# Kernel optimization log

Measured on AMD Instinct MI355X. Metric: run time of the kernel, lower is better.

Reference implementation:

```python
import jax, jax.numpy as jnp
import numpy as np

T, B, E = 2048, 2, 1024
H, R = 16, 8
HD = E // H          # head_dim = 64
VD = E // R          # value_dim = attn_dim // num_rules = 128 (attn_dim = embed_dim)
SEL = E // H         # selection_dim = 64


def _linear_params(key, out_dim, in_dim):
    kw, kb = jax.random.split(key)
    lim = float(np.sqrt(6.0 / (in_dim + out_dim)))  # xavier_uniform
    W = jax.random.uniform(kw, (out_dim, in_dim), jnp.float32, -lim, lim)
    b = jnp.zeros((out_dim,), jnp.float32)
    return W, b


def setup_inputs() -> dict:
    key = jax.random.key(0)
    ks = jax.random.split(key, 7)
    query = jax.random.normal(ks[0], (T, B, E), jnp.float32)
    Wq, bq = _linear_params(ks[1], E, E)
    Wk, bk = _linear_params(ks[2], E, E)
    Wv, bv = _linear_params(ks[3], E, E)          # v_proj: embed_dim -> attn_dim (=E)
    Wvq, bvq = _linear_params(ks[4], SEL * H, E)  # value_q (q_compose=False)
    Wsc, bsc = _linear_params(ks[5], 1, SEL + VD) # score_network (nonlinear=False)
    Wo, bo = _linear_params(ks[6], E, H * VD)     # out_proj
    return {"query": query, "Wq": Wq, "bq": bq, "Wk": Wk, "bk": bk,
            "Wv": Wv, "bv": bv, "Wvq": Wvq, "bvq": bvq,
            "Wsc": Wsc, "bsc": bsc, "Wo": Wo, "bo": bo}


def reference(query, Wq, bq, Wk, bk, Wv, bv, Wvq, bvq, Wsc, bsc, Wo, bo):
    t, b, e = query.shape
    scaling = HD ** -0.5
    # projections (self-attention: k, v from query)
    q = (query @ Wq.T + bq) * scaling                       # (T,B,E)
    k = query @ Wk.T + bk                                   # (T,B,E)
    v = query @ Wv.T + bv                                   # (T,B,attn_dim)
    q = q.reshape(t, b, H, HD).transpose(1, 2, 0, 3)        # (B,H,T,HD)
    k = k.reshape(t, b, H, HD).transpose(1, 2, 0, 3)        # (B,H,S,HD)
    v = v.reshape(t, b, R, VD).transpose(1, 2, 0, 3)        # (B,R,S,VD)
    # standard multi-head search: softmax over source positions
    probs = jax.nn.softmax(jnp.einsum('bhtd,bhsd->bhts', q, k), axis=-1)
    # per-(head, rule) retrieved values
    attn = jnp.einsum('bhts,brsd->bhtrd', probs, v)         # (B,H,T,R,VD)
    # selection query from raw input (q_compose=False)
    v_q = (query @ Wvq.T + bvq).reshape(t, b, H, SEL).transpose(1, 2, 0, 3)  # (B,H,T,SEL)
    v_q = jnp.broadcast_to(v_q[:, :, :, None, :], (b, H, t, R, SEL))
    comp = jnp.concatenate([v_q, attn], axis=-1)            # (B,H,T,R,SEL+VD)
    score = comp @ Wsc.T + bsc                              # (B,H,T,R,1)
    sel = jax.nn.softmax(score, axis=3)                     # softmax over rules
    out = jnp.sum(attn * sel, axis=3)                       # (B,H,T,VD)
    out = out.transpose(2, 0, 1, 3).reshape(t, b, H * VD)   # (T,B,H*VD)
    return out @ Wo.T + bo                                  # (T,B,E)
```

## Files before the change

### kernel.cpp

```cpp
#include <hip/hip_runtime.h>
#include <hip/hip_bf16.h>
#include <stdint.h>

typedef unsigned short u16;
typedef unsigned int u32;
typedef __attribute__((ext_vector_type(8))) short bf16x8;
typedef __attribute__((ext_vector_type(4))) float f32x4;

#define TT 2048
#define BB 2
#define HH 16
#define RR 8
#define SS 2048
#define MROWS 4096

__device__ __forceinline__ float bf2f(u16 h){ union { u32 u; float f; } v; v.u = ((u32)h) << 16; return v.f; }
__device__ __forceinline__ u16 f2bf(float f){ union { float f; u32 u; } v; v.f = f; return (u16)((v.u + 0x7FFFu + ((v.u >> 16) & 1u)) >> 16); }
__device__ __forceinline__ void gl_lds16(const void* g, void* l){
  __builtin_amdgcn_global_load_lds((const __attribute__((address_space(1))) u32*)g,
                                   (__attribute__((address_space(3))) u32*)l, 16, 0, 0);
}

__global__ void k_cvt(const float* __restrict__ s, u16* __restrict__ d, int n, float scale){
  int i = blockIdx.x * blockDim.x + threadIdx.x;
  int st = gridDim.x * blockDim.x;
  for (; i < n; i += st) d[i] = f2bf(s[i] * scale);
}

__global__ void k_bias(const float* __restrict__ bq, const float* __restrict__ bk,
                       const float* __restrict__ bv, float* __restrict__ bb){
  int i = blockIdx.x * blockDim.x + threadIdx.x;
  if (i < 1024){ bb[i] = bq[i] * 0.125f; bb[1024 + i] = bk[i]; bb[2048 + i] = bv[i]; }
}

template<int KD, bool OBF>
__launch_bounds__(256, 2)
__global__ void k_gemm(const u16* __restrict__ A, const u16* __restrict__ Bt,
                       const float* __restrict__ bias, void* __restrict__ Cout, int ldc){
  __shared__ u16 As[128*32];
  __shared__ u16 Bs[128*32];
  const int tid = threadIdx.x, lane = tid & 63, wid = tid >> 6;
  const int mw = wid >> 1, nw = wid & 1;
  const int m0 = blockIdx.y * 128, n0 = blockIdx.x * 128;
  const f32x4 fzero = {0.f, 0.f, 0.f, 0.f};
  f32x4 acc[4][4];
  #pragma unroll
  for (int a = 0; a < 4; ++a)
    #pragma unroll
    for (int c = 0; c < 4; ++c) acc[a][c] = fzero;

  for (int k0 = 0; k0 < KD; k0 += 32){
    #pragma unroll
    for (int it = 0; it < 2; ++it){
      int c = it*256 + tid, r = c >> 2, sl = c & 3;
      gl_lds16(A + (size_t)(m0 + r)*KD + k0 + 8*(sl ^ ((r >> 1) & 3)), &As[c*8]);
    }
    #pragma unroll
    for (int it = 0; it < 2; ++it){
      int c = it*256 + tid, r = c >> 2, sl = c & 3;
      gl_lds16(Bt + (size_t)(n0 + r)*KD + k0 + 8*(sl ^ ((r >> 1) & 3)), &Bs[c*8]);
    }
    __syncthreads();
    bf16x8 af[4], bfr[4];
    #pragma unroll
    for (int mt = 0; mt < 4; ++mt){
      int r = mw*64 + mt*16 + (lane & 15);
      int pos = (lane >> 4) ^ ((r >> 1) & 3);
      af[mt] = *(const bf16x8*)&As[r*32 + pos*8];
    }
    #pragma unroll
    for (int nt = 0; nt < 4; ++nt){
      int r = nw*64 + nt*16 + (lane & 15);
      int pos = (lane >> 4) ^ ((r >> 1) & 3);
      bfr[nt] = *(const bf16x8*)&Bs[r*32 + pos*8];
    }
    #pragma unroll
    for (int mt = 0; mt < 4; ++mt)
      #pragma unroll
      for (int nt = 0; nt < 4; ++nt)
        acc[mt][nt] = __builtin_amdgcn_mfma_f32_16x16x32_bf16(af[mt], bfr[nt], acc[mt][nt], 0, 0, 0);
    __syncthreads();
  }
  #pragma unroll
  for (int nt = 0; nt < 4; ++nt){
    int col = n0 + nw*64 + nt*16 + (lane & 15);
    float bvv = bias[col];
    #pragma unroll
    for (int mt = 0; mt < 4; ++mt)
      #pragma unroll
      for (int j = 0; j < 4; ++j){
        int row = m0 + mw*64 + mt*16 + (lane >> 4)*4 + j;
        float v = acc[mt][nt][j] + bvv;
        if constexpr (OBF) ((u16*)Cout)[(size_t)row*ldc + col] = f2bf(v);
        else               ((float*)Cout)[(size_t)row*ldc + col] = v;
      }
  }
}

__global__ void k_transpose(const u16* __restrict__ qkvb, u16* __restrict__ Vt2){
  __shared__ u16 tile[32][33];
  const int b = blockIdx.z;
  const int s0 = blockIdx.x * 32, n0 = blockIdx.y * 32;
  const int tx = threadIdx.x & 31, ty = threadIdx.x >> 5;
  for (int i = ty; i < 32; i += 8)
    tile[i][tx] = qkvb[(size_t)((s0 + i)*BB + b)*3072 + 2048 + n0 + tx];
  __syncthreads();
  for (int i = ty; i < 32; i += 8){
    int c = n0 + i;
    int nr = ((c & 127) << 3) | (c >> 7);
    Vt2[(size_t)b*1024*SS + (size_t)nr*SS + s0 + tx] = tile[tx][i];
  }
}

__global__ void k_vw2(const u16* __restrict__ qkvb, const float* __restrict__ Wsc,
                      u16* __restrict__ vwa){
  int idx = blockIdx.x * blockDim.x + threadIdx.x;
  if (idx >= BB*16*SS) return;
  int s = idx & (SS - 1);
  int r = (idx >> 11) & 15;
  int b = idx >> 15;
  float a;
  if (r < 8){
    const u16* vrow = qkvb + (size_t)(s*BB + b)*3072 + 2048 + r*128;
    a = 0.f;
    #pragma unroll 8
    for (int d = 0; d < 128; ++d) a += bf2f(vrow[d]) * Wsc[64 + d];
  } else if (r == 8) a = 1.0f;
  else a = 0.f;
  vwa[(size_t)(b*16 + r)*SS + s] = f2bf(a);
}

__launch_bounds__(512, 4)
__global__ void k_attn2(const u16* __restrict__ qkvb, const u16* __restrict__ vwa,
                        u16* __restrict__ probs, float* __restrict__ selp, int bh0){
  __shared__ u16 Qs[64*64];
  __shared__ u16 Ks[128*64];
  __shared__ u16 P[64*136];
  __shared__ float pwL[8][16][16];
  const int tid = threadIdx.x, lane = tid & 63, wid = tid >> 6;
  const int bhl = blockIdx.y;
  const int bh = bh0 + bhl;
  const int t0 = blockIdx.x * 64;
  const int b = bh >> 4, h = bh & 15;
  const u16* qbase = qkvb + b*3072 + h*64;
  const u16* kbase = qkvb + b*3072 + 1024 + h*64;
  const u16* vwbase = vwa + (size_t)b*16*SS;
  u16* pbase = probs + ((size_t)bhl*TT + t0)*SS;
  const f32x4 fzero = {0.f, 0.f, 0.f, 0.f};

  {
    int c = tid, r = c >> 3, sl = c & 7;
    gl_lds16(qbase + (size_t)(t0 + r)*6144 + 8*(sl ^ (r & 7)), &Qs[c*8]);
  }
  __syncthreads();
  bf16x8 qf[4][2];
  #pragma unroll
  for (int mt = 0; mt < 4; ++mt)
    #pragma unroll
    for (int kk = 0; kk < 2; ++kk){
      int r = mt*16 + (lane & 15);
      int pos = (kk*4 + (lane >> 4)) ^ (r & 7);
      qf[mt][kk] = *(const bf16x8*)&Qs[r*64 + pos*8];
    }

  f32x4 pwacc = fzero;
  const int mtp = wid & 3, kks = (wid >> 2)*2;

  for (int s0 = 0; s0 < SS; s0 += 128){
    #pragma unroll
    for (int it = 0; it < 2; ++it){
      int c = it*512 + tid, r = c >> 3, sl = c & 7;
      gl_lds16(kbase + (size_t)(s0 + r)*6144 + 8*(sl ^ (r & 7)), &Ks[c*8]);
    }
    __syncthreads();
    bf16x8 kf[2];
    #pragma unroll
    for (int kk = 0; kk < 2; ++kk){
      int r = wid*16 + (lane & 15);
      int pos = (kk*4 + (lane >> 4)) ^ (r & 7);
      kf[kk] = *(const bf16x8*)&Ks[r*64 + pos*8];
    }
    #pragma unroll
    for (int bt = 0; bt < 4; ++bt){
      f32x4 sa = fzero;
      sa = __builtin_amdgcn_mfma_f32_16x16x32_bf16(kf[0], qf[bt][0], sa, 0, 0, 0);
      sa = __builtin_amdgcn_mfma_f32_16x16x32_bf16(kf[1], qf[bt][1], sa, 0, 0, 0);
      u32 w0 = (u32)f2bf(__expf(sa[0])) | ((u32)f2bf(__expf(sa[1])) << 16);
      u32 w1 = (u32)f2bf(__expf(sa[2])) | ((u32)f2bf(__expf(sa[3])) << 16);
      int t = bt*16 + (lane & 15);
      int sl = wid*16 + (lane >> 4)*4;
      uint2 pk; pk.x = w0; pk.y = w1;
      *(uint2*)&P[t*136 + sl] = pk;
    }
    __syncthreads();
    bf16x8 vwf[2];
    #pragma unroll
    for (int kq = 0; kq < 2; ++kq)
      vwf[kq] = *(const bf16x8*)&vwbase[(size_t)(lane & 15)*SS + s0 + (kks + kq)*32 + (lane >> 4)*8];
    #pragma unroll
    for (int kq = 0; kq < 2; ++kq){
      int kk = kks + kq;
      bf16x8 pa = *(const bf16x8*)&P[(mtp*16 + (lane & 15))*136 + kk*32 + (lane >> 4)*8];
      pwacc = __builtin_amdgcn_mfma_f32_16x16x32_bf16(pa, vwf[kq], pwacc, 0, 0, 0);
    }
    #pragma unroll
    for (int cc = 0; cc < 2; ++cc){
      int c = cc*512 + tid;
      int row = c >> 4, col = c & 15;
      bf16x8 v = *(const bf16x8*)&P[row*136 + col*8];
      *(bf16x8*)&pbase[(size_t)row*SS + s0 + col*8] = v;
    }
  }

  #pragma unroll
  for (int j = 0; j < 4; ++j)
    pwL[wid][(lane >> 4)*4 + j][lane & 15] = pwacc[j];
  __syncthreads();
  if (tid < 64){
    int mt = tid >> 4, tr = tid & 15;
    float pw[9];
    #pragma unroll
    for (int r = 0; r < 9; ++r) pw[r] = pwL[mt][tr][r] + pwL[mt + 4][tr][r];
    float rs = pw[8];
    float inv = 1.0f / rs;
    float mx = -3.0e38f;
    #pragma unroll
    for (int r = 0; r < 8; ++r) mx = fmaxf(mx, pw[r]*inv);
    float e[8], ssum = 0.f;
    #pragma unroll
    for (int r = 0; r < 8; ++r){ e[r] = __expf(pw[r]*inv - mx); ssum += e[r]; }
    #pragma unroll
    for (int r = 0; r < 8; ++r)
      selp[((size_t)bh*TT + t0 + tid)*8 + r] = e[r] / (ssum * rs);
  }
}

__launch_bounds__(256, 2)
__global__ void k_pv3(const u16* __restrict__ probs, const u16* __restrict__ Vt2,
                      const float* __restrict__ selp, u16* __restrict__ oattn,
                      int bh0, int G){
  __shared__ u16 As[128*32];
  __shared__ u16 Bs[128*32];
  const int tid = threadIdx.x, lane = tid & 63, wid = tid >> 6;
  const int mw = wid >> 1, nw = wid & 1;
  int bhl, xy;
  if (G >= 8){
    int fid = blockIdx.x;
    bhl = (fid >> 10)*8 + (fid & 7);
    xy  = (fid >> 3) & 127;
  } else {
    bhl = blockIdx.x >> 7;
    xy  = blockIdx.x & 127;
  }
  const int t0 = (xy >> 3) * 128;
  const int n0 = (xy & 7) * 128;
  const int bh = bh0 + bhl, b = bh >> 4, h = bh & 15;
  const u16* Abase = probs + ((size_t)bhl*TT + t0)*SS;
  const u16* Bbase = Vt2 + (size_t)b*1024*SS + (size_t)n0*SS;
  const f32x4 fzero = {0.f, 0.f, 0.f, 0.f};
  f32x4 acc[4][4];
  #pragma unroll
  for (int a = 0; a < 4; ++a)
    #pragma unroll
    for (int c = 0; c < 4; ++c) acc[a][c] = fzero;

  for (int k0 = 0; k0 < SS; k0 += 32){
    #pragma unroll
    for (int it = 0; it < 2; ++it){
      int c = it*256 + tid, r = c >> 2, sl = c & 3;
      gl_lds16(Abase + (size_t)r*SS + k0 + 8*(sl ^ ((r >> 1) & 3)), &As[c*8]);
    }
    #pragma unroll
    for (int it = 0; it < 2; ++it){
      int c = it*256 + tid, r = c >> 2, sl = c & 3;
      gl_lds16(Bbase + (size_t)r*SS + k0 + 8*(sl ^ ((r >> 1) & 3)), &Bs[c*8]);
    }
    __syncthreads();
    bf16x8 af[4], bfr[4];
    #pragma unroll
    for (int mt = 0; mt < 4; ++mt){
      int r = mw*64 + mt*16 + (lane & 15);
      int pos = (lane >> 4) ^ ((r >> 1) & 3);
      af[mt] = *(const bf16x8*)&As[r*32 + pos*8];
    }
    #pragma unroll
    for (int nt = 0; nt < 4; ++nt){
      int r = nw*64 + nt*16 + (lane & 15);
      int pos = (lane >> 4) ^ ((r >> 1) & 3);
      bfr[nt] = *(const bf16x8*)&Bs[r*32 + pos*8];
    }
    #pragma unroll
    for (int mt = 0; mt < 4; ++mt)
      #pragma unroll
      for (int nt = 0; nt < 4; ++nt)
        acc[mt][nt] = __builtin_amdgcn_mfma_f32_16x16x32_bf16(af[mt], bfr[nt], acc[mt][nt], 0, 0, 0);
    __syncthreads();
  }

  const int c15 = lane & 15, g = lane >> 4, r8 = c15 & 7;
  float sel[4][4];
  #pragma unroll
  for (int mt = 0; mt < 4; ++mt)
    #pragma unroll
    for (int j = 0; j < 4; ++j){
      int trow = t0 + mw*64 + mt*16 + g*4 + j;
      sel[mt][j] = selp[((size_t)bh*TT + trow)*8 + r8];
    }
  #pragma unroll
  for (int mt = 0; mt < 4; ++mt)
    #pragma unroll
    for (int nt = 0; nt < 4; ++nt){
      float v0 = acc[mt][nt][0] * sel[mt][0];
      float v1 = acc[mt][nt][1] * sel[mt][1];
      float v2 = acc[mt][nt][2] * sel[mt][2];
      float v3 = acc[mt][nt][3] * sel[mt][3];
      #pragma unroll
      for (int mask = 1; mask < 8; mask <<= 1){
        v0 += __shfl_xor(v0, mask, 64);
        v1 += __shfl_xor(v1, mask, 64);
        v2 += __shfl_xor(v2, mask, 64);
        v3 += __shfl_xor(v3, mask, 64);
      }
      if (r8 == 0){
        int dglob = (n0 >> 3) + nw*8 + nt*2 + (c15 >> 3);
        int tb = t0 + mw*64 + mt*16 + g*4;
        u16* dst = oattn + (size_t)(tb*BB + b)*2048 + h*128 + dglob;
        dst[0*BB*2048] = f2bf(v0);
        dst[1*BB*2048] = f2bf(v1);
        dst[2*BB*2048] = f2bf(v2);
        dst[3*BB*2048] = f2bf(v3);
      }
    }
}

extern "C" void kernel_launch(void* const* d_in, const int* in_sizes, int n_in,
                              void* d_out, int out_size, void* d_ws, size_t ws_size,
                              hipStream_t stream){
  (void)in_sizes; (void)n_in;
  const float* query = (const float*)d_in[0];
  const float* Wq  = (const float*)d_in[1];
  const float* bq  = (const float*)d_in[2];
  const float* Wk  = (const float*)d_in[3];
  const float* bk  = (const float*)d_in[4];
  const float* Wv  = (const float*)d_in[5];
  const float* bv  = (const float*)d_in[6];
  const float* Wsc = (const float*)d_in[9];
  const float* Wo  = (const float*)d_in[11];
  const float* bo  = (const float*)d_in[12];

  char* p = (char*)d_ws;
  auto carve = [&](size_t bytes) -> char* {
    char* r = p; p += (bytes + 255) & ~((size_t)255); return r;
  };
  u16*   Xb     = (u16*)  carve((size_t)MROWS*1024*2);
  u16*   Wb     = (u16*)  carve((size_t)3072*1024*2);
  u16*   Wob    = (u16*)  carve((size_t)1024*2048*2);
  float* bb     = (float*)carve(3072*4);
  u16*   qkvb   = (u16*)  carve((size_t)MROWS*3072*2);
  u16*   Vt2    = (u16*)  carve((size_t)BB*1024*SS*2);
  u16*   vwa    = (u16*)  carve((size_t)BB*16*SS*2);
  u16*   oattn  = (u16*)  carve((size_t)MROWS*2048*2);
  float* selp   = (float*)carve((size_t)32*TT*RR*4);
  size_t fixed = (size_t)(p - (char*)d_ws);
  int G = 32;
  while (G > 1 && fixed + ((size_t)G*TT*SS*2 + 256) > ws_size) G >>= 1;
  u16* probs;
  if (fixed + ((size_t)G*TT*SS*2 + 256) <= ws_size){
    probs = (u16*)carve((size_t)G*TT*SS*2);
  } else {
    G = 1;
    probs = Xb;
  }

  k_cvt<<<1024, 256, 0, stream>>>(query, Xb, MROWS*1024, 1.0f);
  k_cvt<<<512, 256, 0, stream>>>(Wq, Wb, 1024*1024, 0.125f);
  k_cvt<<<512, 256, 0, stream>>>(Wk, Wb + 1024*1024, 1024*1024, 1.0f);
  k_cvt<<<512, 256, 0, stream>>>(Wv, Wb + 2*1024*1024, 1024*1024, 1.0f);
  k_cvt<<<1024, 256, 0, stream>>>(Wo, Wob, 1024*2048, 1.0f);
  k_bias<<<4, 256, 0, stream>>>(bq, bk, bv, bb);
  k_gemm<1024, true><<<dim3(24, 32), 256, 0, stream>>>(Xb, Wb, bb, qkvb, 3072);
  k_transpose<<<dim3(64, 32, 2), 256, 0, stream>>>(qkvb, Vt2);
  k_vw2<<<256, 256, 0, stream>>>(qkvb, Wsc, vwa);
  for (int bh0 = 0; bh0 < 32; bh0 += G){
    k_attn2<<<dim3(32, G), 512, 0, stream>>>(qkvb, vwa, probs, selp, bh0);
    k_pv3<<<G*128, 256, 0, stream>>>(probs, Vt2, selp, oattn, bh0, G);
  }
  k_gemm<2048, false><<<dim3(8, 32), 256, 0, stream>>>(oattn, Wob, bo, d_out, 1024);
}
```

Baseline: 500.6 us.

## Use 256x256 tiles with 4-stage LDS prefetch pipeline in PV GEMM

Replaces the PV kernel with a 512-thread version computing 256x256 output tiles. It uses a 4-deep LDS ring buffer that prefetches K-slices three iterations ahead, with explicit vmcnt waits and a single barrier per step. MFMA blocks are split into two halves with priority raising so B-fragment loads overlap compute. Larger tiles cut global traffic per FLOP, but the 128KB LDS footprint limits occupancy to one block per CU.

After: 437.0 us. 12.7% less time.

```diff
diff --git a/kernel.cpp b/kernel.cpp
--- a/kernel.cpp
+++ b/kernel.cpp
@@ -235,85 +235,112 @@
   }
 }
 
-__launch_bounds__(256, 2)
-__global__ void k_pv3(const u16* __restrict__ probs, const u16* __restrict__ Vt2,
+__launch_bounds__(512, 2)
+__global__ void k_pv4(const u16* __restrict__ probs, const u16* __restrict__ Vt2,
                       const float* __restrict__ selp, u16* __restrict__ oattn,
                       int bh0, int G){
-  __shared__ u16 As[128*32];
-  __shared__ u16 Bs[128*32];
+  __shared__ u16 L[4*16384];
   const int tid = threadIdx.x, lane = tid & 63, wid = tid >> 6;
-  const int mw = wid >> 1, nw = wid & 1;
-  int bhl, xy;
-  if (G >= 8){
-    int fid = blockIdx.x;
-    bhl = (fid >> 10)*8 + (fid & 7);
-    xy  = (fid >> 3) & 127;
-  } else {
-    bhl = blockIdx.x >> 7;
-    xy  = blockIdx.x & 127;
-  }
-  const int t0 = (xy >> 3) * 128;
-  const int n0 = (xy & 7) * 128;
+  const int mw = wid & 1, nw2 = wid >> 1;
+  int fid = blockIdx.x, bhl, xy;
+  if (G >= 8){ bhl = (fid & 7) + 8*(fid >> 8); xy = (fid >> 3) & 31; }
+  else       { bhl = fid >> 5;                 xy = fid & 31; }
+  const int t0 = (xy >> 2) * 256;
+  const int n0 = (xy & 3) * 256;
   const int bh = bh0 + bhl, b = bh >> 4, h = bh & 15;
   const u16* Abase = probs + ((size_t)bhl*TT + t0)*SS;
   const u16* Bbase = Vt2 + (size_t)b*1024*SS + (size_t)n0*SS;
   const f32x4 fzero = {0.f, 0.f, 0.f, 0.f};
-  f32x4 acc[4][4];
-  #pragma unroll
-  for (int a = 0; a < 4; ++a)
+  f32x4 acc[8][4];
+  #pragma unroll
+  for (int a = 0; a < 8; ++a)
     #pragma unroll
     for (int c = 0; c < 4; ++c) acc[a][c] = fzero;
 
-  for (int k0 = 0; k0 < SS; k0 += 32){
-    #pragma unroll
-    for (int it = 0; it < 2; ++it){
-      int c = it*256 + tid, r = c >> 2, sl = c & 3;
-      gl_lds16(Abase + (size_t)r*SS + k0 + 8*(sl ^ ((r >> 1) & 3)), &As[c*8]);
-    }
-    #pragma unroll
-    for (int it = 0; it < 2; ++it){
-      int c = it*256 + tid, r = c >> 2, sl = c & 3;
-      gl_lds16(Bbase + (size_t)r*SS + k0 + 8*(sl ^ ((r >> 1) & 3)), &Bs[c*8]);
-    }
-    __syncthreads();
-    bf16x8 af[4], bfr[4];
-    #pragma unroll
-    for (int mt = 0; mt < 4; ++mt){
-      int r = mw*64 + mt*16 + (lane & 15);
+  auto stage = [&](int q){
+    u16* As = &L[(q & 3) * 16384];
+    u16* Bs = As + 8192;
+    #pragma unroll
+    for (int i = 0; i < 2; ++i){
+      int ci = i*512 + tid, r = ci >> 2, sl = ci & 3;
+      gl_lds16(Abase + (size_t)r*SS + q*32 + 8*(sl ^ ((r >> 1) & 3)), &As[ci*8]);
+    }
+    #pragma unroll
+    for (int i = 0; i < 2; ++i){
+      int ci = i*512 + tid, r = ci >> 2, sl = ci & 3;
+      gl_lds16(Bbase + (size_t)r*SS + q*32 + 8*(sl ^ ((r >> 1) & 3)), &Bs[ci*8]);
+    }
+  };
+
+  stage(0); stage(1); stage(2);
+  asm volatile("s_waitcnt vmcnt(8)" ::: "memory");
+  __builtin_amdgcn_s_barrier();
+
+  for (int q = 0; q < 64; ++q){
+    const u16* As = &L[(q & 3) * 16384];
+    const u16* Bs = As + 8192;
+    bf16x8 af[8], bf0[2];
+    #pragma unroll
+    for (int mf = 0; mf < 8; ++mf){
+      int r = mw*128 + mf*16 + (lane & 15);
       int pos = (lane >> 4) ^ ((r >> 1) & 3);
-      af[mt] = *(const bf16x8*)&As[r*32 + pos*8];
-    }
-    #pragma unroll
-    for (int nt = 0; nt < 4; ++nt){
-      int r = nw*64 + nt*16 + (lane & 15);
+      af[mf] = *(const bf16x8*)&As[r*32 + pos*8];
+    }
+    #pragma unroll
+    for (int nf = 0; nf < 2; ++nf){
+      int r = nw2*64 + nf*16 + (lane & 15);
       int pos = (lane >> 4) ^ ((r >> 1) & 3);
-      bfr[nt] = *(const bf16x8*)&Bs[r*32 + pos*8];
-    }
-    #pragma unroll
-    for (int mt = 0; mt < 4; ++mt)
-      #pragma unroll
-      for (int nt = 0; nt < 4; ++nt)
-        acc[mt][nt] = __builtin_amdgcn_mfma_f32_16x16x32_bf16(af[mt], bfr[nt], acc[mt][nt], 0, 0, 0);
-    __syncthreads();
+      bf0[nf] = *(const bf16x8*)&Bs[r*32 + pos*8];
+    }
+    if (q + 3 < 64) stage(q + 3);
+    asm volatile("s_waitcnt lgkmcnt(0)" ::: "memory");
+    __builtin_amdgcn_sched_barrier(0);
+    __builtin_amdgcn_s_setprio(1);
+    #pragma unroll
+    for (int mf = 0; mf < 8; ++mf){
+      acc[mf][0] = __builtin_amdgcn_mfma_f32_16x16x32_bf16(af[mf], bf0[0], acc[mf][0], 0, 0, 0);
+      acc[mf][1] = __builtin_amdgcn_mfma_f32_16x16x32_bf16(af[mf], bf0[1], acc[mf][1], 0, 0, 0);
+    }
+    __builtin_amdgcn_s_setprio(0);
+    bf16x8 bf1[2];
+    #pragma unroll
+    for (int nf = 0; nf < 2; ++nf){
+      int r = nw2*64 + 32 + nf*16 + (lane & 15);
+      int pos = (lane >> 4) ^ ((r >> 1) & 3);
+      bf1[nf] = *(const bf16x8*)&Bs[r*32 + pos*8];
+    }
+    asm volatile("s_waitcnt lgkmcnt(0)" ::: "memory");
+    __builtin_amdgcn_sched_barrier(0);
+    __builtin_amdgcn_s_setprio(1);
+    #pragma unroll
+    for (int mf = 0; mf < 8; ++mf){
+      acc[mf][2] = __builtin_amdgcn_mfma_f32_16x16x32_bf16(af[mf], bf1[0], acc[mf][2], 0, 0, 0);
+      acc[mf][3] = __builtin_amdgcn_mfma_f32_16x16x32_bf16(af[mf], bf1[1], acc[mf][3], 0, 0, 0);
+    }
+    __builtin_amdgcn_s_setprio(0);
+    if (q < 61)       asm volatile("s_waitcnt vmcnt(8)" ::: "memory");
+    else if (q == 61) asm volatile("s_waitcnt vmcnt(4)" ::: "memory");
+    else              asm volatile("s_waitcnt vmcnt(0)" ::: "memory");
+    __builtin_amdgcn_s_barrier();
   }
 
   const int c15 = lane & 15, g = lane >> 4, r8 = c15 & 7;
-  float sel[4][4];
-  #pragma unroll
-  for (int mt = 0; mt < 4; ++mt)
+  float sel[8][4];
+  #pragma unroll
+  for (int mf = 0; mf < 8; ++mf)
     #pragma unroll
     for (int j = 0; j < 4; ++j){
-      int trow = t0 + mw*64 + mt*16 + g*4 + j;
-      sel[mt][j] = selp[((size_t)bh*TT + trow)*8 + r8];
-    }
-  #pragma unroll
-  for (int mt = 0; mt < 4; ++mt)
-    #pragma unroll
-    for (int nt = 0; nt < 4; ++nt){
-      float v0 = acc[mt][nt][0] * sel[mt][0];
-      float v1 = acc[mt][nt][1] * sel[mt][1];
-      float v2 = acc[mt][nt][2] * sel[mt][2];
-      float v3 = acc[mt][nt][3] * sel[mt][3];
+      int trow = t0 + mw*128 + mf*16 + g*4 + j;
+      sel[mf][j] = selp[((size_t)bh*TT + trow)*8 + r8];
+    }
+  #pragma unroll
+  for (int mf = 0; mf < 8; ++mf)
+    #pragma unroll
+    for (int nf = 0; nf < 4; ++nf){
+      float v0 = acc[mf][nf][0] * sel[mf][0];
+      float v1 = acc[mf][nf][1] * sel[mf][1];
+      float v2 = acc[mf][nf][2] * sel[mf][2];
+      float v3 = acc[mf][nf][3] * sel[mf][3];
       #pragma unroll
       for (int mask = 1; mask < 8; mask <<= 1){
         v0 += __shfl_xor(v0, mask, 64);
@@ -322,8 +349,8 @@
         v3 += __shfl_xor(v3, mask, 64);
       }
       if (r8 == 0){
-        int dglob = (n0 >> 3) + nw*8 + nt*2 + (c15 >> 3);
-        int tb = t0 + mw*64 + mt*16 + g*4;
+        int dglob = (n0 >> 3) + nw2*8 + nf*2 + (c15 >> 3);
+        int tb = t0 + mw*128 + mf*16 + g*4;
         u16* dst = oattn + (size_t)(tb*BB + b)*2048 + h*128 + dglob;
         dst[0*BB*2048] = f2bf(v0);
         dst[1*BB*2048] = f2bf(v1);
@@ -383,7 +410,7 @@
   k_vw2<<<256, 256, 0, stream>>>(qkvb, Wsc, vwa);
   for (int bh0 = 0; bh0 < 32; bh0 += G){
     k_attn2<<<dim3(32, G), 512, 0, stream>>>(qkvb, vwa, probs, selp, bh0);
-    k_pv3<<<G*128, 256, 0, stream>>>(probs, Vt2, selp, oattn, bh0, G);
+    k_pv4<<<G*32, 512, 0, stream>>>(probs, Vt2, selp, oattn, bh0, G);
   }
   k_gemm<2048, false><<<dim3(8, 32), 256, 0, stream>>>(oattn, Wob, bo, d_out, 1024);
 }
```
